# Kernel tuning notes

Hardware: AMD Instinct MI355X
Metric: run time of the kernel (lower is better)

The kernel has to match this reference:

```python
import jax, jax.numpy as jnp
import numpy as np

N = 100000   # nodes
E = 1600000  # edges (avg degree 16)
D = 128      # in_dim
H = 128      # hidden_dim
C = 40       # n_classes
L = 3        # n_layers


def setup_inputs() -> dict:
    key = jax.random.key(0)
    ks = jax.random.split(key, 10)
    x = jax.random.normal(ks[0], (N, D), jnp.float32)
    adj = jax.random.randint(ks[1], (2, E), 0, N, jnp.int32)
    adj_b = jax.random.randint(ks[2], (2, E), 0, N, jnp.int32)
    perm = jax.random.randint(ks[3], (N,), 0, N, jnp.int32)
    mix_ratio = jax.random.uniform(ks[4], (), jnp.float32)
    Wl = jax.random.normal(ks[5], (L, D, H), jnp.float32) / jnp.sqrt(D)
    bl = jnp.zeros((L, H), jnp.float32)
    Wr = jax.random.normal(ks[6], (L, D, H), jnp.float32) / jnp.sqrt(D)
    W_out = jax.random.normal(ks[7], (H, C), jnp.float32) / jnp.sqrt(H)
    b_out = jnp.zeros((C,), jnp.float32)
    return {"x": x, "Wl": Wl, "bl": bl, "Wr": Wr, "W_out": W_out,
            "b_out": b_out, "mix_ratio": mix_ratio, "adj": adj,
            "adj_b": adj_b, "perm": perm}


def _sage(x_src, x_dst, edge, Wl_i, bl_i, Wr_i):
    # PyG SAGEConv: out = lin_l(mean_{j->i} x_src[j]) + lin_r(x_dst[i])
    src, dst = edge[0], edge[1]
    msg = x_src[src]                                            # [E, d] gather
    agg = jax.ops.segment_sum(msg, dst, num_segments=x_dst.shape[0])
    deg = jax.ops.segment_sum(jnp.ones((edge.shape[1],), x_src.dtype), dst,
                              num_segments=x_dst.shape[0])
    agg = agg / jnp.maximum(deg, 1.0)[:, None]                  # mean aggregation
    return agg @ Wl_i + bl_i + x_dst @ Wr_i


def reference(x, Wl, bl, Wr, W_out, b_out, mix_ratio, adj, adj_b, perm):
    r = mix_ratio
    # pre-aggregation passes (dropout inactive / eval math, no batch_norm)
    aggr = [x]
    for i in range(L - 1):
        aggr.append(jax.nn.relu(_sage(aggr[-1], aggr[-1], adj, Wl[i], bl[i], Wr[i])))
    aggr_b = [h[perm] for h in aggr]
    # mixup blend and dual-branch propagation
    x_mix = aggr[0] * r + aggr_b[0] * (1.0 - r)
    for i in range(L):
        x_new = jax.nn.relu(_sage(aggr[i], x_mix, adj, Wl[i], bl[i], Wr[i]))
        x_new_b = jax.nn.relu(_sage(aggr_b[i], x_mix, adj_b, Wl[i], bl[i], Wr[i]))
        x_mix = x_new * r + x_new_b * (1.0 - r)
    logits = x_mix @ W_out + b_out
    return jax.nn.log_softmax(logits, axis=-1)
```

## Files before the change

### kernel.cpp

```cpp
#include <hip/hip_runtime.h>
#include <math.h>

#define N_NODES 100000
#define N_EDGES 1600000
#define DIM 128
#define NCLS 40
#define NSHARD 8
#define SHARD_SZ (N_NODES / NSHARD)
#define CAP 64

typedef unsigned short u16;
typedef unsigned int u32;
typedef unsigned char u8;
typedef __attribute__((ext_vector_type(8))) short bf16x8;
typedef __attribute__((ext_vector_type(4))) float f32x4;
typedef __attribute__((ext_vector_type(2))) float f32x2;

union Frag { bf16x8 v; u16 u[8]; uint4 ui; };

__device__ __forceinline__ float b2f_lo(u32 u){ union{u32 i;float f;}c; c.i=u<<16; return c.f; }
__device__ __forceinline__ float b2f_hi(u32 u){ union{u32 i;float f;}c; c.i=u&0xffff0000u; return c.f; }
__device__ __forceinline__ u16 f2b(float f){ union{float f;u32 i;}c; c.f=f; u32 r=c.i+0x7fffu+((c.i>>16)&1u); return (u16)(r>>16); }

__device__ __forceinline__ u32 pack4_fp8(float a, float b, float c, float d) {
    u32 v = 0;
    v = __builtin_amdgcn_cvt_pk_fp8_f32(a, b, v, false);
    v = __builtin_amdgcn_cvt_pk_fp8_f32(c, d, v, true);
    return v;
}
__device__ __forceinline__ void addq(float* a, u32 w) {
    f32x2 p0 = __builtin_amdgcn_cvt_pk_f32_fp8(w, false);
    f32x2 p1 = __builtin_amdgcn_cvt_pk_f32_fp8(w, true);
    a[0] += p0.x; a[1] += p0.y; a[2] += p1.x; a[3] += p1.y;
}

__global__ void scatter_pad(const int* __restrict__ adjA, const int* __restrict__ adjB,
        int* __restrict__ cntA, int* __restrict__ cntB,
        int* __restrict__ ssA, int* __restrict__ ssB,
        const int* __restrict__ perm, int E) {
    const int cls = blockIdx.x & 7;
    const int lo = cls * SHARD_SZ, hi = lo + SHARD_SZ;
    int i = (blockIdx.x >> 3) * blockDim.x + threadIdx.x;
    if (i < E) {
        int d = adjA[E + i];
        if (d >= lo && d < hi) {
            int p = atomicAdd(&cntA[d], 1);
            if (p < CAP) ssA[d * CAP + p] = adjA[i];
        }
    } else {
        i -= E;
        if (i < E) {
            int d = adjB[E + i];
            if (d >= lo && d < hi) {
                int p = atomicAdd(&cntB[d], 1);
                if (p < CAP) ssB[d * CAP + p] = perm[adjB[i]];
            }
        }
    }
}

__global__ void conv_mix(const float* __restrict__ x, const int* __restrict__ perm,
                         const float* __restrict__ rp, u16* __restrict__ xb,
                         u16* __restrict__ xm, u8* __restrict__ xq) {
    int i = (blockIdx.x * 256 + threadIdx.x) * 4;
    int n = i >> 7, f = i & 127;
    float r = *rp;
    int p = perm[n];
    float4 xv = *(const float4*)(x + i);
    float4 pv = *(const float4*)(x + (size_t)p * DIM + f);
    ushort4 b, m;
    b.x = f2b(xv.x); b.y = f2b(xv.y); b.z = f2b(xv.z); b.w = f2b(xv.w);
    m.x = f2b(r * xv.x + (1.f - r) * pv.x);
    m.y = f2b(r * xv.y + (1.f - r) * pv.y);
    m.z = f2b(r * xv.z + (1.f - r) * pv.z);
    m.w = f2b(r * xv.w + (1.f - r) * pv.w);
    *(ushort4*)(xb + i) = b;
    *(ushort4*)(xm + i) = m;
    *(u32*)(xq + i) = pack4_fp8(xv.x, xv.y, xv.z, xv.w);
}

__global__ void pack_weights(const float* __restrict__ Wl, const float* __restrict__ Wr,
                             u16* __restrict__ WlP, u16* __restrict__ WrP) {
    int i = blockIdx.x * 256 + threadIdx.x;
    int layer = i >> 14, idx = i & 16383;
    int j = idx & 7, l = (idx >> 3) & 63, t = (idx >> 9) & 3, c = idx >> 11;
    int k = ((t >> 1) << 6) + (((l >> 4)) << 4) + ((t & 1) << 3) + j;
    int col = (c << 4) + (l & 15);
    WlP[i] = f2b(Wl[layer * 16384 + k * DIM + col]);
    WrP[i] = f2b(Wr[layer * 16384 + k * DIM + col]);
}


__device__ __forceinline__ void gather_frags_q(const u8* __restrict__ src,
        const int* __restrict__ lst, int deg, int q, Frag* f) {
    float acc[32];
    #pragma unroll
    for (int j = 0; j < 32; ++j) acc[j] = 0.f;
    const u8* s0 = src + q * 16;
    const u8* s1 = src + 64 + q * 16;
    int d = deg > CAP ? CAP : deg;
    #pragma unroll 4
    for (int e = 0; e < d; ++e) {
        int s = lst[e];
        uint4 v0 = *(const uint4*)(s0 + (size_t)s * DIM);
        uint4 v1 = *(const uint4*)(s1 + (size_t)s * DIM);
        addq(acc +  0, v0.x); addq(acc +  4, v0.y);
        addq(acc +  8, v0.z); addq(acc + 12, v0.w);
        addq(acc + 16, v1.x); addq(acc + 20, v1.y);
        addq(acc + 24, v1.z); addq(acc + 28, v1.w);
    }
    float inv = (deg > 0) ? 1.f / (float)deg : 0.f;
    #pragma unroll
    for (int t = 0; t < 4; ++t)
        #pragma unroll
        for (int j = 0; j < 8; ++j) f[t].u[j] = f2b(acc[t * 8 + j] * inv);
}

__device__ __forceinline__ void load_frags(const u16* __restrict__ row, int q, Frag* f) {
    const u16* p = row + q * 16;
    f[0].ui = *(const uint4*)(p);
    f[1].ui = *(const uint4*)(p + 8);
    f[2].ui = *(const uint4*)(p + 64);
    f[3].ui = *(const uint4*)(p + 72);
}

__device__ __forceinline__ void load_frags_q8(const u8* __restrict__ row, int q, Frag* f) {
    const u8* p = row + q * 16;
    uint4 v0 = *(const uint4*)(p);
    uint4 v1 = *(const uint4*)(p + 64);
    float a[32];
    #pragma unroll
    for (int j = 0; j < 32; ++j) a[j] = 0.f;
    addq(a +  0, v0.x); addq(a +  4, v0.y); addq(a +  8, v0.z); addq(a + 12, v0.w);
    addq(a + 16, v1.x); addq(a + 20, v1.y); addq(a + 24, v1.z); addq(a + 28, v1.w);
    #pragma unroll
    for (int t = 0; t < 4; ++t)
        #pragma unroll
        for (int j = 0; j < 8; ++j) f[t].u[j] = f2b(a[t * 8 + j]);
}

template<int XMODE>
__global__ __launch_bounds__(256) void sage_layer(
        const u8* __restrict__ srcq, const u16* __restrict__ srcb,
        const u16* __restrict__ xm,
        const int* __restrict__ cnt_a, const int* __restrict__ ss_a,
        const int* __restrict__ cnt_b, const int* __restrict__ ss_b,
        const u16* __restrict__ WlP, const u16* __restrict__ WrP,
        const float* __restrict__ bl, const float* __restrict__ rp,
        u8* __restrict__ Aqout, u16* __restrict__ xmout)
{
    const int lane = threadIdx.x & 63;
    const int wave = threadIdx.x >> 6;
    const int nb = blockIdx.x * 64 + wave * 16;
    const int m = lane & 15, q = lane >> 4;
    const int n = nb + m;
    const bool vld = n < N_NODES;
    const int nc = vld ? n : N_NODES - 1;

    Frag fA[4], fB[4], fX[4], fM[4];
    gather_frags_q(srcq, ss_a + (size_t)nc * CAP, cnt_a[nc], q, fA);
    gather_frags_q(srcq, ss_b + (size_t)nc * CAP, cnt_b[nc], q, fB);
    if (XMODE == 1) load_frags(srcb + (size_t)nc * DIM, q, fX);
    if (XMODE == 2) load_frags_q8(srcq + (size_t)nc * DIM, q, fX);
    load_frags(xm + (size_t)nc * DIM, q, fM);
    float r = *rp;

    const int col = m;
    const int rowb = q * 4;
    for (int c = 0; c < 8; ++c) {
        Frag wl[4], wr[4];
        #pragma unroll
        for (int t = 0; t < 4; ++t) {
            wl[t].ui = *(const uint4*)(WlP + ((c * 4 + t) * 64 + lane) * 8);
            wr[t].ui = *(const uint4*)(WrP + ((c * 4 + t) * 64 + lane) * 8);
        }
        f32x4 u = {0.f, 0.f, 0.f, 0.f};
        #pragma unroll
        for (int t = 0; t < 4; ++t)
            u = __builtin_amdgcn_mfma_f32_16x16x32_bf16(fA[t].v, wl[t].v, u, 0, 0, 0);
        f32x4 s = {0.f, 0.f, 0.f, 0.f};
        #pragma unroll
        for (int t = 0; t < 4; ++t)
            s = __builtin_amdgcn_mfma_f32_16x16x32_bf16(fM[t].v, wr[t].v, s, 0, 0, 0);
        f32x4 pb = s;
        #pragma unroll
        for (int t = 0; t < 4; ++t)
            pb = __builtin_amdgcn_mfma_f32_16x16x32_bf16(fB[t].v, wl[t].v, pb, 0, 0, 0);
        f32x4 aA;
        if (XMODE != 0) {
            aA = u;
            #pragma unroll
            for (int t = 0; t < 4; ++t)
                aA = __builtin_amdgcn_mfma_f32_16x16x32_bf16(fX[t].v, wr[t].v, aA, 0, 0, 0);
        }
        f32x4 pa = u + s;
        float bias = bl[c * 16 + col];
        #pragma unroll
        for (int r2 = 0; r2 < 4; ++r2) {
            int nr = nb + rowb + r2;
            if (nr < N_NODES) {
                if (XMODE != 0) {
                    float v = fmaxf(aA[r2] + bias, 0.f);
                    u32 q8 = 0;
                    q8 = __builtin_amdgcn_cvt_pk_fp8_f32(v, v, q8, false);
                    Aqout[(size_t)nr * DIM + c * 16 + col] = (u8)(q8 & 0xff);
                }
                float va = fmaxf(pa[r2] + bias, 0.f);
                float vb = fmaxf(pb[r2] + bias, 0.f);
                xmout[(size_t)nr * DIM + c * 16 + col] = f2b(r * va + (1.f - r) * vb);
            }
        }
    }
}

__device__ __forceinline__ void load_row(const u16* __restrict__ row, int lane,
                                         float* __restrict__ ldsrow) {
    u32 v = *(const u32*)(row + lane * 2);
    ldsrow[lane * 2]     = b2f_lo(v);
    ldsrow[lane * 2 + 1] = b2f_hi(v);
}

__global__ __launch_bounds__(256) void out_kernel(const u16* __restrict__ xm,
        const float* __restrict__ Wo, const float* __restrict__ bo,
        float* __restrict__ out) {
    __shared__ float row[4][DIM];
    const int wave = threadIdx.x >> 6;
    const int lane = threadIdx.x & 63;
    const int n = blockIdx.x * 4 + wave;
    load_row(xm + (size_t)n * DIM, lane, row[wave]);
    float acc = -1e30f;
    if (lane < NCLS) {
        acc = bo[lane];
        #pragma unroll 4
        for (int k = 0; k < DIM; ++k) acc += row[wave][k] * Wo[k * NCLS + lane];
    }
    float mx = acc;
    for (int o = 32; o > 0; o >>= 1) mx = fmaxf(mx, __shfl_xor(mx, o, 64));
    float e = (lane < NCLS) ? expf(acc - mx) : 0.f;
    float sum = e;
    for (int o = 32; o > 0; o >>= 1) sum += __shfl_xor(sum, o, 64);
    if (lane < NCLS) out[(size_t)n * NCLS + lane] = acc - mx - logf(sum);
}


extern "C" void kernel_launch(void* const* d_in, const int* in_sizes, int n_in,
                              void* d_out, int out_size, void* d_ws, size_t ws_size,
                              hipStream_t stream) {
    const float* x    = (const float*)d_in[0];
    const float* Wl   = (const float*)d_in[1];
    const float* bl   = (const float*)d_in[2];
    const float* Wr   = (const float*)d_in[3];
    const float* Wo   = (const float*)d_in[4];
    const float* bo   = (const float*)d_in[5];
    const float* rp   = (const float*)d_in[6];
    const int*   adj  = (const int*)d_in[7];
    const int*   adjb = (const int*)d_in[8];
    const int*   perm = (const int*)d_in[9];
    float* out = (float*)d_out;

    char* ws = (char*)d_ws;
    size_t off = 0;
    auto alloc = [&](size_t bytes) {
        char* p = ws + off;
        off += (bytes + 255) & ~(size_t)255;
        return p;
    };
    int* cur2   = (int*)alloc((size_t)2 * N_NODES * 4);
    int* ss_a   = (int*)alloc((size_t)N_NODES * CAP * 4);
    int* ss_b   = (int*)alloc((size_t)N_NODES * CAP * 4);
    u16* WlP    = (u16*)alloc(3 * 16384 * 2);
    u16* WrP    = (u16*)alloc(3 * 16384 * 2);
    const size_t FB = (size_t)N_NODES * DIM * 2;
    const size_t QB = (size_t)N_NODES * DIM;
    u16* xb  = (u16*)alloc(FB);
    u16* xm0 = (u16*)alloc(FB);
    u16* xm1 = (u16*)alloc(FB);
    u8*  xq  = (u8*)alloc(QB);
    u8*  A1q = (u8*)alloc(QB);
    u16* xm2 = xb;
    u8*  A2q = (u8*)xm0;
    u16* xm3 = xm1;
    int* cntA = cur2, *cntB = cur2 + N_NODES;

    const int nbE = (N_EDGES + 255) / 256;

    hipMemsetAsync(cur2, 0, (size_t)2 * N_NODES * 4, stream);
    scatter_pad<<<NSHARD * 2 * nbE, 256, 0, stream>>>(adj, adjb, cntA, cntB,
                                                      ss_a, ss_b, perm, N_EDGES);

    pack_weights<<<192, 256, 0, stream>>>(Wl, Wr, WlP, WrP);
    conv_mix<<<(N_NODES * DIM) / 1024, 256, 0, stream>>>(x, perm, rp, xb, xm0, xq);

    const int WP = 16384;
    const int nbS = (N_NODES + 63) / 64;

    sage_layer<1><<<nbS, 256, 0, stream>>>(xq, xb, xm0,
        cntA, ss_a, cntB, ss_b, WlP, WrP, bl, rp, A1q, xm1);
    sage_layer<2><<<nbS, 256, 0, stream>>>(A1q, nullptr, xm1,
        cntA, ss_a, cntB, ss_b, WlP + WP, WrP + WP, bl + DIM, rp, A2q, xm2);
    sage_layer<0><<<nbS, 256, 0, stream>>>(A2q, nullptr, xm2,
        cntA, ss_a, cntB, ss_b, WlP + 2 * WP, WrP + 2 * WP, bl + 2 * DIM, rp,
        nullptr, xm3);

    out_kernel<<<N_NODES / 4, 256, 0, stream>>>(xm3, Wo, bo, out);
}
```

Before: 745.1 us.

## Replace sharded scatter with two-pass bucketed edge compaction and drop bf16 x copy

Edge bucketing now runs in two passes. The first pass reads each edge once and uses wave-aggregated atomics to append (src,dst) pairs into per-shard, per-replica segments. The second pass scatters those segments into the padded neighbor lists, replacing the old kernel that re-read all edges eight times (once per shard). The first layer now reads the self features from the fp8 copy instead of a separate bf16 copy, which removes one conversion write and one buffer. This adds a workspace segment buffer with a fixed capacity, lowers first-layer self-term precision, and could drop edges if a bucket overflows.

New measurement: 1.264 ms. 1.7x slower.

```diff
diff --git a/kernel.cpp b/kernel.cpp
--- a/kernel.cpp
+++ b/kernel.cpp
@@ -8,10 +8,13 @@
 #define NSHARD 8
 #define SHARD_SZ (N_NODES / NSHARD)
 #define CAP 64
+#define NREP 32
+#define CAPSEG 8192
 
 typedef unsigned short u16;
 typedef unsigned int u32;
 typedef unsigned char u8;
+typedef unsigned long long u64;
 typedef __attribute__((ext_vector_type(8))) short bf16x8;
 typedef __attribute__((ext_vector_type(4))) float f32x4;
 typedef __attribute__((ext_vector_type(2))) float f32x2;
@@ -34,33 +37,59 @@
     a[0] += p0.x; a[1] += p0.y; a[2] += p1.x; a[3] += p1.y;
 }
 
-__global__ void scatter_pad(const int* __restrict__ adjA, const int* __restrict__ adjB,
-        int* __restrict__ cntA, int* __restrict__ cntB,
-        int* __restrict__ ssA, int* __restrict__ ssB,
-        const int* __restrict__ perm, int E) {
-    const int cls = blockIdx.x & 7;
-    const int lo = cls * SHARD_SZ, hi = lo + SHARD_SZ;
-    int i = (blockIdx.x >> 3) * blockDim.x + threadIdx.x;
-    if (i < E) {
-        int d = adjA[E + i];
-        if (d >= lo && d < hi) {
-            int p = atomicAdd(&cntA[d], 1);
-            if (p < CAP) ssA[d * CAP + p] = adjA[i];
+__global__ void compact_edges(const int* __restrict__ adjA, const int* __restrict__ adjB,
+                              const int* __restrict__ perm,
+                              int* __restrict__ cur, int2* __restrict__ seg, int E) {
+    const int nbE = E / 256;
+    const int g = blockIdx.x >= nbE;
+    const int e = (blockIdx.x - g * nbE) * 256 + threadIdx.x;
+    const int* adjG = g ? adjB : adjA;
+    int src = adjG[e];
+    int dst = adjG[E + e];
+    if (g) src = perm[src];
+    const int cls = (u32)dst / SHARD_SZ;
+    const int lane = threadIdx.x & 63;
+    const u64 ltmask = (1ull << lane) - 1;
+    const int r = blockIdx.x & (NREP - 1);
+    #pragma unroll
+    for (int c = 0; c < 8; ++c) {
+        u64 mask = __ballot(cls == c);
+        if (mask == 0) continue;
+        int leader = __ffsll(mask) - 1;
+        int base = 0;
+        int idx = (g * 8 + c) * NREP + r;
+        if (lane == leader) base = atomicAdd(&cur[idx], (int)__popcll(mask));
+        base = __shfl(base, leader, 64);
+        if (cls == c) {
+            int off = base + (int)__popcll(mask & ltmask);
+            if (off < CAPSEG) seg[(size_t)idx * CAPSEG + off] = make_int2(src, dst);
         }
-    } else {
-        i -= E;
-        if (i < E) {
-            int d = adjB[E + i];
-            if (d >= lo && d < hi) {
-                int p = atomicAdd(&cntB[d], 1);
-                if (p < CAP) ssB[d * CAP + p] = perm[adjB[i]];
-            }
-        }
+    }
+}
+
+__global__ void scatter_pad2(const int2* __restrict__ seg, const int* __restrict__ cur,
+                             int* __restrict__ cntA, int* __restrict__ cntB,
+                             int* __restrict__ ssA, int* __restrict__ ssB) {
+    const int c = blockIdx.x & 7;
+    const int t = blockIdx.x >> 3;
+    const int r = t & (NREP - 1);
+    const int g = (t >> 5) & 1;
+    const int chunk = t >> 6;
+    const int idx = (g * 8 + c) * NREP + r;
+    int n = cur[idx];
+    if (n > CAPSEG) n = CAPSEG;
+    const int2* s = seg + (size_t)idx * CAPSEG;
+    int* cnt = g ? cntB : cntA;
+    int* ss  = g ? ssB  : ssA;
+    for (int i = chunk * 256 + threadIdx.x; i < n; i += 1024) {
+        int2 p = s[i];
+        int pos = atomicAdd(&cnt[p.y], 1);
+        if (pos < CAP) ss[p.y * CAP + pos] = p.x;
     }
 }
 
 __global__ void conv_mix(const float* __restrict__ x, const int* __restrict__ perm,
-                         const float* __restrict__ rp, u16* __restrict__ xb,
+                         const float* __restrict__ rp,
                          u16* __restrict__ xm, u8* __restrict__ xq) {
     int i = (blockIdx.x * 256 + threadIdx.x) * 4;
     int n = i >> 7, f = i & 127;
@@ -68,13 +97,11 @@
     int p = perm[n];
     float4 xv = *(const float4*)(x + i);
     float4 pv = *(const float4*)(x + (size_t)p * DIM + f);
-    ushort4 b, m;
-    b.x = f2b(xv.x); b.y = f2b(xv.y); b.z = f2b(xv.z); b.w = f2b(xv.w);
+    ushort4 m;
     m.x = f2b(r * xv.x + (1.f - r) * pv.x);
     m.y = f2b(r * xv.y + (1.f - r) * pv.y);
     m.z = f2b(r * xv.z + (1.f - r) * pv.z);
     m.w = f2b(r * xv.w + (1.f - r) * pv.w);
-    *(ushort4*)(xb + i) = b;
     *(ushort4*)(xm + i) = m;
     *(u32*)(xq + i) = pack4_fp8(xv.x, xv.y, xv.z, xv.w);
 }
@@ -89,7 +116,6 @@
     WlP[i] = f2b(Wl[layer * 16384 + k * DIM + col]);
     WrP[i] = f2b(Wr[layer * 16384 + k * DIM + col]);
 }
-
 
 __device__ __forceinline__ void gather_frags_q(const u8* __restrict__ src,
         const int* __restrict__ lst, int deg, int q, Frag* f) {
@@ -141,8 +167,7 @@
 
 template<int XMODE>
 __global__ __launch_bounds__(256) void sage_layer(
-        const u8* __restrict__ srcq, const u16* __restrict__ srcb,
-        const u16* __restrict__ xm,
+        const u8* __restrict__ srcq, const u16* __restrict__ xm,
         const int* __restrict__ cnt_a, const int* __restrict__ ss_a,
         const int* __restrict__ cnt_b, const int* __restrict__ ss_b,
         const u16* __restrict__ WlP, const u16* __restrict__ WrP,
@@ -160,7 +185,6 @@
     Frag fA[4], fB[4], fX[4], fM[4];
     gather_frags_q(srcq, ss_a + (size_t)nc * CAP, cnt_a[nc], q, fA);
     gather_frags_q(srcq, ss_b + (size_t)nc * CAP, cnt_b[nc], q, fB);
-    if (XMODE == 1) load_frags(srcb + (size_t)nc * DIM, q, fX);
     if (XMODE == 2) load_frags_q8(srcq + (size_t)nc * DIM, q, fX);
     load_frags(xm + (size_t)nc * DIM, q, fM);
     float r = *rp;
@@ -265,40 +289,42 @@
         off += (bytes + 255) & ~(size_t)255;
         return p;
     };
-    int* cur2   = (int*)alloc((size_t)2 * N_NODES * 4);
-    int* ss_a   = (int*)alloc((size_t)N_NODES * CAP * 4);
-    int* ss_b   = (int*)alloc((size_t)N_NODES * CAP * 4);
-    u16* WlP    = (u16*)alloc(3 * 16384 * 2);
-    u16* WrP    = (u16*)alloc(3 * 16384 * 2);
+    int*  cnt2 = (int*)alloc(((size_t)2 * N_NODES + 512) * 4);
+    int*  ss_a = (int*)alloc((size_t)N_NODES * CAP * 4);
+    int*  ss_b = (int*)alloc((size_t)N_NODES * CAP * 4);
+    int2* seg  = (int2*)alloc((size_t)2 * 8 * NREP * CAPSEG * 8);
+    u16*  WlP  = (u16*)alloc(3 * 16384 * 2);
+    u16*  WrP  = (u16*)alloc(3 * 16384 * 2);
     const size_t FB = (size_t)N_NODES * DIM * 2;
     const size_t QB = (size_t)N_NODES * DIM;
-    u16* xb  = (u16*)alloc(FB);
     u16* xm0 = (u16*)alloc(FB);
     u16* xm1 = (u16*)alloc(FB);
     u8*  xq  = (u8*)alloc(QB);
     u8*  A1q = (u8*)alloc(QB);
-    u16* xm2 = xb;
-    u8*  A2q = (u8*)xm0;
+    u16* xm2 = xm0;
+    u8*  A2q = xq;
     u16* xm3 = xm1;
-    int* cntA = cur2, *cntB = cur2 + N_NODES;
-
-    const int nbE = (N_EDGES + 255) / 256;
-
-    hipMemsetAsync(cur2, 0, (size_t)2 * N_NODES * 4, stream);
-    scatter_pad<<<NSHARD * 2 * nbE, 256, 0, stream>>>(adj, adjb, cntA, cntB,
-                                                      ss_a, ss_b, perm, N_EDGES);
+    int* cntA = cnt2, *cntB = cnt2 + N_NODES;
+    int* cur  = cnt2 + 2 * N_NODES;
+
+    const int nbE = N_EDGES / 256;
+
+    hipMemsetAsync(cnt2, 0, ((size_t)2 * N_NODES + 512) * 4, stream);
+
+    compact_edges<<<2 * nbE, 256, 0, stream>>>(adj, adjb, perm, cur, seg, N_EDGES);
+    scatter_pad2<<<8 * 256, 256, 0, stream>>>(seg, cur, cntA, cntB, ss_a, ss_b);
 
     pack_weights<<<192, 256, 0, stream>>>(Wl, Wr, WlP, WrP);
-    conv_mix<<<(N_NODES * DIM) / 1024, 256, 0, stream>>>(x, perm, rp, xb, xm0, xq);
+    conv_mix<<<(N_NODES * DIM) / 1024, 256, 0, stream>>>(x, perm, rp, xm0, xq);
 
     const int WP = 16384;
     const int nbS = (N_NODES + 63) / 64;
 
-    sage_layer<1><<<nbS, 256, 0, stream>>>(xq, xb, xm0,
+    sage_layer<2><<<nbS, 256, 0, stream>>>(xq, xm0,
         cntA, ss_a, cntB, ss_b, WlP, WrP, bl, rp, A1q, xm1);
-    sage_layer<2><<<nbS, 256, 0, stream>>>(A1q, nullptr, xm1,
+    sage_layer<2><<<nbS, 256, 0, stream>>>(A1q, xm1,
         cntA, ss_a, cntB, ss_b, WlP + WP, WrP + WP, bl + DIM, rp, A2q, xm2);
-    sage_layer<0><<<nbS, 256, 0, stream>>>(A2q, nullptr, xm2,
+    sage_layer<0><<<nbS, 256, 0, stream>>>(A2q, xm2,
         cntA, ss_a, cntB, ss_b, WlP + 2 * WP, WrP + 2 * WP, bl + 2 * DIM, rp,
         nullptr, xm3);
 
```
